# Performance work log

Hardware: AMD Instinct MI355X
Metric: run time of the kernel (lower is better)

Reference implementation:

```python
import jax, jax.numpy as jnp
import numpy as np

NUM_OCTAVES = 6
LN_EPS = 1e-5


def layer_norm(x, scale, bias):
    mu = jnp.mean(x, axis=-1, keepdims=True)
    var = jnp.var(x, axis=-1, keepdims=True)
    return (x - mu) * jax.lax.rsqrt(var + LN_EPS) * scale + bias


def bilinear_sample(img, xy):
    """torch.grid_sample(mode='bilinear', align_corners=False, padding='zeros').
    img: [B,C,H,W], xy: [B,N,2] with (x,y) in [-1,1]. Returns [B,N,C]."""
    B, C, H, W = img.shape
    ix = ((xy[..., 0] + 1.0) * W - 1.0) * 0.5  # [B,N] pixel-space x
    iy = ((xy[..., 1] + 1.0) * H - 1.0) * 0.5
    x0 = jnp.floor(ix)
    y0 = jnp.floor(iy)
    wx1 = ix - x0
    wy1 = iy - y0

    def corner(xc, yc, w):
        valid = (xc >= 0) & (xc < W) & (yc >= 0) & (yc < H)
        xi = jnp.clip(xc, 0, W - 1).astype(jnp.int32)
        yi = jnp.clip(yc, 0, H - 1).astype(jnp.int32)
        vals = jax.vmap(lambda im, a, b: im[:, a, b])(img, yi, xi)  # [B,C,N]
        return vals * (w * valid.astype(img.dtype))[:, None, :]

    out = (corner(x0, y0, (1 - wx1) * (1 - wy1))
           + corner(x0 + 1, y0, wx1 * (1 - wy1))
           + corner(x0, y0 + 1, (1 - wx1) * wy1)
           + corner(x0 + 1, y0 + 1, wx1 * wy1))
    return out.transpose(0, 2, 1)  # [B,N,C]


def pos_enc(c):
    # SRT-style positional encoding: sin/cos at octaves 2^o * pi, o in [0, NUM_OCTAVES)
    octs = (2.0 ** jnp.arange(NUM_OCTAVES)) * jnp.pi  # [O]
    s = c[..., None] * octs  # [B,N,2,O]
    B, N = c.shape[:2]
    return jnp.concatenate([jnp.sin(s).reshape(B, N, -1), jnp.cos(s).reshape(B, N, -1)], axis=-1)


def reference(image, latents, coords, ln_q_scale, ln_q_bias, ln_c_scale, ln_c_bias, w_q, w_kv, w_out, b_out):
    B, C, H, W = latents.shape
    N = coords.shape[1]  # must equal H*W when feat_unfold
    xy = jnp.flip(coords, axis=-1)  # coords.flip(-1): (row,col) -> (x,y)

    # q_features = grid_sample(latents)
    q_features = bilinear_sample(latents, xy)  # [B,N,C]

    # --- feature unfold: faithful raw reshape (B,N,C) -> (B,C,H,W) as in source ---
    uf = q_features.reshape(B, C, H, W)
    rows = jnp.arange(H)
    cols = jnp.arange(W)
    nbrs = []
    for i in (-1, 0, 1):
        for j in (-1, 0, 1):
            vr = jnp.clip(rows + i, 0, H - 1)
            vc = jnp.clip(cols + j, 0, W - 1)
            nbrs.append(uf[:, :, vr[:, None], vc[None, :]])  # [B,C,H,W]
    ctx = jnp.stack(nbrs, axis=1).reshape(B, 9, C, H * W).transpose(0, 3, 1, 2)  # [B,N,9,C]

    # --- PreNorm(Attention): per-point 1-query attention over 9-neighbor context ---
    xq = layer_norm(q_features, ln_q_scale, ln_q_bias)[:, :, None, :]  # [B,N,1,C]
    cn = layer_norm(ctx, ln_c_scale, ln_c_bias)                        # [B,N,9,C]
    q = xq @ w_q                                                       # [B,N,1,C]
    kv = cn @ w_kv                                                     # [B,N,9,2C]
    k, v = kv[..., :C], kv[..., C:]
    sim = jnp.einsum('bnqc,bnkc->bnqk', q, k) * (C ** -0.5)
    attn = jax.nn.softmax(sim, axis=-1)
    o = jnp.einsum('bnqk,bnkc->bnqc', attn, v)
    q_features = (o @ w_out + b_out)[:, :, 0, :]  # [B,N,C] (DropPath is identity at eval)

    # --- q_coords = grid_sample(make_coord grid) ---
    fy = -1.0 + (2.0 * jnp.arange(H) + 1.0) / H
    fx = -1.0 + (2.0 * jnp.arange(W) + 1.0) / W
    fcoord = jnp.stack(jnp.meshgrid(fy, fx, indexing='ij'), axis=0)  # [2,H,W]
    fcoord = jnp.broadcast_to(fcoord[None], (B, 2, H, W)).astype(latents.dtype)
    q_coords = bilinear_sample(fcoord, xy)  # [B,N,2]

    # --- q_input = grid_sample(image) ---
    q_input = bilinear_sample(image, xy)  # [B,N,1]

    pe = pos_enc((q_coords + 1.0) * 0.5)  # [B,N,4*NUM_OCTAVES]
    return jnp.concatenate([q_features, q_input, pe], axis=-1)


def setup_inputs() -> dict:
    key = jax.random.key(0)
    ks = jax.random.split(key, 8)
    B, C, H, W = 4, 64, 128, 128
    N = H * W
    image = jax.random.normal(ks[0], (B, 1, 256, 256), dtype=jnp.float32)
    latents = jax.random.normal(ks[1], (B, C, H, W), dtype=jnp.float32)
    coords = jax.random.uniform(ks[2], (B, N, 2), dtype=jnp.float32, minval=-1.0, maxval=1.0)
    w_q = jax.random.normal(ks[3], (C, C), dtype=jnp.float32) * (C ** -0.5)
    w_kv = jax.random.normal(ks[4], (C, 2 * C), dtype=jnp.float32) * (C ** -0.5)
    w_out = jax.random.normal(ks[5], (C, C), dtype=jnp.float32) * (C ** -0.5)
    return {
        'image': image, 'latents': latents, 'coords': coords,
        'ln_q_scale': jnp.ones((C,), jnp.float32), 'ln_q_bias': jnp.zeros((C,), jnp.float32),
        'ln_c_scale': jnp.ones((C,), jnp.float32), 'ln_c_bias': jnp.zeros((C,), jnp.float32),
        'w_q': w_q, 'w_kv': w_kv, 'w_out': w_out, 'b_out': jnp.zeros((C,), jnp.float32),
    }
```

## Files before the change

kernel.cpp:

```cpp
#include <hip/hip_runtime.h>
#include <cstdint>


typedef __attribute__((ext_vector_type(8))) short bf16x8;
typedef __attribute__((ext_vector_type(4))) float f32x4;
typedef __attribute__((ext_vector_type(4))) uint32_t u32x4;
typedef __attribute__((ext_vector_type(2))) uint32_t u32x2;

__device__ __forceinline__ float wsum(float v){
#pragma unroll
  for(int o=32;o>0;o>>=1) v += __shfl_xor(v,o,64);
  return v;
}
__device__ __forceinline__ unsigned short f2bf(float x){
  union{float f; uint32_t u;} c; c.f=x;
  uint32_t r = c.u + 0x7fffu + ((c.u>>16)&1u);
  return (unsigned short)(r>>16);
}
__device__ __forceinline__ float bf2f(unsigned short h){
  union{uint32_t u; float f;} c; c.u = ((uint32_t)h)<<16; return c.f;
}
__device__ __forceinline__ float blo(uint32_t u){
  union{uint32_t x; float f;} c; c.x = u<<16; return c.f;
}
__device__ __forceinline__ float bhi(uint32_t u){
  union{uint32_t x; float f;} c; c.x = u & 0xffff0000u; return c.f;
}

__global__ __launch_bounds__(256) void k_tr_bf(const float* __restrict__ in,
                                               uint16_t* __restrict__ out){
  __shared__ float t[64][65];
  const int b  = blockIdx.y;
  const int p0 = blockIdx.x * 64;
  const float* src = in  + (size_t)b * (64 * 16384);
  uint16_t*    dst = out + (size_t)b * (64 * 16384);
  const int tx = threadIdx.x & 63, ty = threadIdx.x >> 6;
#pragma unroll
  for(int j=0;j<16;j++){ int r = ty + j*4; t[r][tx] = src[(size_t)r*16384 + p0 + tx]; }
  __syncthreads();
#pragma unroll
  for(int j=0;j<16;j++){ int pr = ty + j*4; dst[(size_t)(p0+pr)*64 + tx] = f2bf(t[tx][pr]); }
}

__global__ __launch_bounds__(256) void k_sample(const uint16_t* __restrict__ lat_t,
                                                const float* __restrict__ coords,
                                                const float* __restrict__ image,
                                                const float* __restrict__ lsq,
                                                const float* __restrict__ lbq,
                                                uint16_t* __restrict__ qf,
                                                uint32_t* __restrict__ xq,
                                                float* __restrict__ out){
  const int lane = threadIdx.x & 63;
  const int pidx = blockIdx.x * 4 + (threadIdx.x >> 6);
  const int b = pidx >> 14;
  const float y = coords[(size_t)pidx*2 + 0];
  const float x = coords[(size_t)pidx*2 + 1];

  float ix = ((x + 1.f)*128.f - 1.f)*0.5f;
  float iy = ((y + 1.f)*128.f - 1.f)*0.5f;
  float x0 = floorf(ix), y0 = floorf(iy);
  float wx1 = ix - x0, wy1 = iy - y0;
  float acc = 0.f, qcy = 0.f, qcx = 0.f;
  const uint16_t* latb = lat_t + (size_t)b*16384*64;
#pragma unroll
  for(int cy=0; cy<2; cy++){
#pragma unroll
    for(int cx=0; cx<2; cx++){
      int xi = (int)x0 + cx, yi = (int)y0 + cy;
      float w = (cx ? wx1 : 1.f-wx1) * (cy ? wy1 : 1.f-wy1);
      bool valid = (xi>=0)&&(xi<128)&&(yi>=0)&&(yi<128);
      float wv = valid ? w : 0.f;
      int xc = min(max(xi,0),127), yc = min(max(yi,0),127);
      acc += wv * bf2f(latb[(size_t)(yc*128 + xc)*64 + lane]);
      qcy += wv * (-1.f + (2.f*(float)yc + 1.f)*(1.f/128.f));
      qcx += wv * (-1.f + (2.f*(float)xc + 1.f)*(1.f/128.f));
    }
  }
  qf[(size_t)pidx*64 + lane] = f2bf(acc);

  float s1 = wsum(acc), s2 = wsum(acc*acc);
  float mu = s1*(1.f/64.f);
  float rs = rsqrtf(s2*(1.f/64.f) - mu*mu + 1e-5f);
  float xv = (acc - mu)*rs*lsq[lane] + lbq[lane];
  float va = __shfl(xv, (lane&31)*2), vb = __shfl(xv, (lane&31)*2+1);
  if(lane < 32)
    xq[(size_t)pidx*32 + (lane ^ ((pidx&7)<<2))] = ((uint32_t)f2bf(vb)<<16) | f2bf(va);

  float jx = ((x + 1.f)*256.f - 1.f)*0.5f;
  float jy = ((y + 1.f)*256.f - 1.f)*0.5f;
  float jx0 = floorf(jx), jy0 = floorf(jy);
  float ux1 = jx - jx0, uy1 = jy - jy0;
  float acc2 = 0.f;
  const float* imb = image + (size_t)b*256*256;
#pragma unroll
  for(int cy=0; cy<2; cy++){
#pragma unroll
    for(int cx=0; cx<2; cx++){
      int xi = (int)jx0 + cx, yi = (int)jy0 + cy;
      float w = (cx ? ux1 : 1.f-ux1) * (cy ? uy1 : 1.f-uy1);
      bool valid = (xi>=0)&&(xi<256)&&(yi>=0)&&(yi<256);
      int xc = min(max(xi,0),255), yc = min(max(yi,0),255);
      acc2 += (valid ? w : 0.f) * imb[yc*256 + xc];
    }
  }
  size_t obase = (size_t)pidx * 89;
  if(lane == 0) out[obase + 64] = acc2;

  if(lane < 24){
    int r = (lane < 12) ? lane : lane - 12;
    int d = r / 6, o = r % 6;
    float cval = (d == 0) ? qcy : qcx;
    cval = (cval + 1.f) * 0.5f;
    float arg = cval * 3.14159265358979323846f * (float)(1 << o);
    out[obase + 65 + lane] = (lane < 12) ? sinf(arg) : cosf(arg);
  }
}

__global__ __launch_bounds__(256) void k_tr_ln(const uint16_t* __restrict__ qf,
                                               const float* __restrict__ lsc,
                                               const float* __restrict__ lbc,
                                               uint32_t* __restrict__ cn){
  __shared__ float t[64][65];
  const int b  = blockIdx.y;
  const int p0 = blockIdx.x * 64;
  const uint16_t* src = qf + (size_t)b * 1048576;
  const int tx = threadIdx.x & 63, ty = threadIdx.x >> 6;
  const float sc = lsc[tx], bc = lbc[tx];
#pragma unroll
  for(int j=0;j<16;j++){ int r = ty + j*4; t[r][tx] = bf2f(src[(size_t)r*16384 + p0 + tx]); }
  __syncthreads();
#pragma unroll
  for(int j=0;j<16;j++){
    int pr = ty + j*4;
    float v = t[tx][pr];
    float s1 = wsum(v), s2 = wsum(v*v);
    float mu = s1*(1.f/64.f);
    float rs = rsqrtf(s2*(1.f/64.f) - mu*mu + 1e-5f);
    float cv = (v - mu)*rs*sc + bc;
    float va = __shfl(cv, (tx&31)*2), vb = __shfl(cv, (tx&31)*2+1);
    int rown = p0 + pr;
    size_t row = (size_t)b*16384 + rown;
    if(tx < 32)
      cn[row*32 + (tx ^ ((rown&7)<<2))] = ((uint32_t)f2bf(vb)<<16) | f2bf(va);
  }
}

template<int MODE>
__global__ __launch_bounds__(256) void k_gemm(const uint32_t* A, const float* W,
                                              const float* bias,
                                              uint16_t* oK, uint16_t* oV, float* oF){
  constexpr int N  = (MODE==1) ? 128 : 64;
  constexpr int NT = (MODE==1) ? 2 : 1;
  __shared__ uint32_t la[128*32];
  const int t  = threadIdx.x;
  const int wv = t >> 6, ln = t & 63;
  const uint32_t* src = A + (size_t)blockIdx.x * 4096;
#pragma unroll
  for(int i=0;i<4;i++){
    *(u32x4*)&la[(i*256+t)*4] = *(const u32x4*)&src[(i*256+t)*4];
  }
  bf16x8 bfr[NT][2];
#pragma unroll
  for(int nt=0;nt<NT;nt++){
    const int ntg = wv*NT + nt;
#pragma unroll
    for(int ks=0;ks<2;ks++){
#pragma unroll
      for(int e=0;e<8;e++){
        int k = ks*32 + (ln>>4)*8 + e;
        bfr[nt][ks][e] = (short)f2bf(W[(size_t)k*N + ntg*16 + (ln&15)]);
      }
    }
  }
  __syncthreads();

  f32x4 acc[8][NT];
#pragma unroll
  for(int m=0;m<8;m++)
#pragma unroll
    for(int nt=0;nt<NT;nt++) acc[m][nt] = (f32x4){0.f,0.f,0.f,0.f};

#pragma unroll
  for(int m=0;m<8;m++){
    const int R = m*16 + (ln&15);
#pragma unroll
    for(int ks=0;ks<2;ks++){
      const int gs = (ks*4 + (ln>>4)) ^ (R&7);
      bf16x8 af = *(const bf16x8*)&la[R*32 + gs*4];
#pragma unroll
      for(int nt=0;nt<NT;nt++)
        acc[m][nt] = __builtin_amdgcn_mfma_f32_16x16x32_bf16(af, bfr[nt][ks], acc[m][nt], 0,0,0);
    }
  }

  const size_t r0 = (size_t)blockIdx.x * 128;
#pragma unroll
  for(int m=0;m<8;m++){
#pragma unroll
    for(int nt=0;nt<NT;nt++){
      const int ntg = wv*NT + nt;
      const int col = ntg*16 + (ln&15);
#pragma unroll
      for(int r=0;r<4;r++){
        const size_t row = r0 + m*16 + (ln>>4)*4 + r;
        float v = acc[m][nt][r];
        if constexpr (MODE==0){
          oK[row*64 + col] = f2bf(v * 0.125f);
        } else if constexpr (MODE==1){
          if(col < 64) oK[row*64 + col]      = f2bf(v);
          else         oV[row*64 + (col-64)] = f2bf(v);
        } else {
          oF[row*89 + col] = v + bias[col];
        }
      }
    }
  }
}

__global__ __launch_bounds__(256) void k_attn3(const uint16_t* __restrict__ Qb,
                                               const uint16_t* __restrict__ Kb,
                                               const uint16_t* __restrict__ Vb,
                                               uint32_t* __restrict__ O){
  const int t  = threadIdx.x;
  const int ln = t & 63;
  const int cl = ln & 15;
  const int p  = blockIdx.x*16 + (t>>6)*4 + (ln>>4);
  const int b = p >> 14, n = p & 16383, h = n >> 7, w = n & 127;

  u32x2 qp = *(const u32x2*)((const char*)Qb + (size_t)p*128 + cl*8);
  const float q0 = blo(qp.x), q1 = bhi(qp.x), q2 = blo(qp.y), q3 = bhi(qp.y);

  const size_t base = (size_t)b * 16384;
  float sim[9];
  uint32_t v01[9], v23[9];
#pragma unroll
  for(int k=0;k<9;k++){
    int hh = min(max(h + k/3 - 1, 0), 127);
    int ww = min(max(w + k%3 - 1, 0), 127);
    size_t pos = base + hh*128 + ww;
    u32x2 kp = *(const u32x2*)((const char*)Kb + pos*128 + cl*8);
    u32x2 vp = *(const u32x2*)((const char*)Vb + pos*128 + cl*8);
    v01[k] = vp.x; v23[k] = vp.y;
    float s = q0*blo(kp.x) + q1*bhi(kp.x) + q2*blo(kp.y) + q3*bhi(kp.y);
#pragma unroll
    for(int o=8;o>0;o>>=1) s += __shfl_xor(s, o, 64);
    sim[k] = s;
  }
  float m = sim[0];
#pragma unroll
  for(int k=1;k<9;k++) m = fmaxf(m, sim[k]);
  float se = 0.f, o0 = 0.f, o1 = 0.f, o2 = 0.f, o3 = 0.f;
#pragma unroll
  for(int k=0;k<9;k++){
    float e = __expf(sim[k] - m);
    se += e;
    o0 += e*blo(v01[k]); o1 += e*bhi(v01[k]);
    o2 += e*blo(v23[k]); o3 += e*bhi(v23[k]);
  }
  float inv = 1.f/se;
  o0 *= inv; o1 *= inv; o2 *= inv; o3 *= inv;
  const uint32_t w01 = ((uint32_t)f2bf(o1)<<16) | f2bf(o0);
  const uint32_t w23 = ((uint32_t)f2bf(o3)<<16) | f2bf(o2);
  const int key = (p&7)<<2;
  O[(size_t)p*32 + ((cl*2  ) ^ key)] = w01;
  O[(size_t)p*32 + ((cl*2+1) ^ key)] = w23;
}

extern "C" void kernel_launch(void* const* d_in, const int* in_sizes, int n_in,
                              void* d_out, int out_size, void* d_ws, size_t ws_size,
                              hipStream_t stream){
  const float* image   = (const float*)d_in[0];
  const float* latents = (const float*)d_in[1];
  const float* coords  = (const float*)d_in[2];
  const float* lsq     = (const float*)d_in[3];
  const float* lbq     = (const float*)d_in[4];
  const float* lsc     = (const float*)d_in[5];
  const float* lbc     = (const float*)d_in[6];
  const float* wq      = (const float*)d_in[7];
  const float* wkv     = (const float*)d_in[8];
  const float* wout    = (const float*)d_in[9];
  const float* bout    = (const float*)d_in[10];
  float* out = (float*)d_out;

  char* ws = (char*)d_ws;
  uint16_t* latT = (uint16_t*)ws;
  uint32_t* CN   = (uint32_t*)ws;
  uint16_t* Kb   = (uint16_t*)ws;
  uint16_t* Vb   = (uint16_t*)(ws + 8388608);
  uint16_t* qfB  = (uint16_t*)(ws + 16777216);
  uint32_t* O    = (uint32_t*)(ws + 16777216);
  uint32_t* XQ   = (uint32_t*)(ws + 25165824);
  uint16_t* Qb   = (uint16_t*)(ws + 25165824);

  dim3 trg(256, 4);
  k_tr_bf <<<trg,   256, 0, stream>>>(latents, latT);
  k_sample<<<16384, 256, 0, stream>>>(latT, coords, image, lsq, lbq, qfB, XQ, out);
  k_tr_ln <<<trg,   256, 0, stream>>>(qfB, lsc, lbc, CN);
  k_gemm<0><<<512,  256, 0, stream>>>(XQ, wq,  nullptr, Qb, nullptr, nullptr);
  k_gemm<1><<<512,  256, 0, stream>>>(CN, wkv, nullptr, Kb, Vb,      nullptr);
  k_attn3 <<<4096,  256, 0, stream>>>(Qb, Kb, Vb, O);
  k_gemm<2><<<512,  256, 0, stream>>>(O, wout, bout, nullptr, nullptr, out);
}
```

Before: 168.9 us.

## Fuse context layernorm with Q/KV projections and attention with output projection

Merges the transpose+LayerNorm kernel and the two projection GEMMs into one kernel that keeps the normalized context and query tiles in shared memory. It also merges the 3x3 neighborhood attention with the output projection, so the attention result stays in LDS instead of going through global memory. This cuts the pipeline from seven launches to four and removes the CN and O intermediate round trips. The trade-off is larger shared-memory footprint, more registers per block and fewer blocks for the attention stage, since 512 blocks of 512 threads replace 4096 blocks of 256.

```diff
diff --git a/kernel.cpp b/kernel.cpp
--- a/kernel.cpp
+++ b/kernel.cpp
@@ -4,6 +4,7 @@
 
 typedef __attribute__((ext_vector_type(8))) short bf16x8;
 typedef __attribute__((ext_vector_type(4))) float f32x4;
+typedef __attribute__((ext_vector_type(2))) float f32x2;
 typedef __attribute__((ext_vector_type(4))) uint32_t u32x4;
 typedef __attribute__((ext_vector_type(2))) uint32_t u32x2;
 
@@ -116,154 +117,245 @@
   }
 }
 
-__global__ __launch_bounds__(256) void k_tr_ln(const uint16_t* __restrict__ qf,
-                                               const float* __restrict__ lsc,
-                                               const float* __restrict__ lbc,
-                                               uint32_t* __restrict__ cn){
-  __shared__ float t[64][65];
-  const int b  = blockIdx.y;
-  const int p0 = blockIdx.x * 64;
-  const uint16_t* src = qf + (size_t)b * 1048576;
-  const int tx = threadIdx.x & 63, ty = threadIdx.x >> 6;
-  const float sc = lsc[tx], bc = lbc[tx];
-#pragma unroll
-  for(int j=0;j<16;j++){ int r = ty + j*4; t[r][tx] = bf2f(src[(size_t)r*16384 + p0 + tx]); }
-  __syncthreads();
-#pragma unroll
-  for(int j=0;j<16;j++){
-    int pr = ty + j*4;
-    float v = t[tx][pr];
-    float s1 = wsum(v), s2 = wsum(v*v);
-    float mu = s1*(1.f/64.f);
-    float rs = rsqrtf(s2*(1.f/64.f) - mu*mu + 1e-5f);
-    float cv = (v - mu)*rs*sc + bc;
-    float va = __shfl(cv, (tx&31)*2), vb = __shfl(cv, (tx&31)*2+1);
-    int rown = p0 + pr;
-    size_t row = (size_t)b*16384 + rown;
-    if(tx < 32)
-      cn[row*32 + (tx ^ ((rown&7)<<2))] = ((uint32_t)f2bf(vb)<<16) | f2bf(va);
-  }
-}
-
-template<int MODE>
-__global__ __launch_bounds__(256) void k_gemm(const uint32_t* A, const float* W,
-                                              const float* bias,
-                                              uint16_t* oK, uint16_t* oV, float* oF){
-  constexpr int N  = (MODE==1) ? 128 : 64;
-  constexpr int NT = (MODE==1) ? 2 : 1;
-  __shared__ uint32_t la[128*32];
+__global__ __launch_bounds__(256) void k_proj(const uint16_t* __restrict__ qf,
+                                              const uint32_t* __restrict__ XQ,
+                                              const float* __restrict__ lsc,
+                                              const float* __restrict__ lbc,
+                                              const float* __restrict__ wq,
+                                              const float* __restrict__ wkv,
+                                              uint16_t* __restrict__ Qb,
+                                              uint16_t* __restrict__ Kb,
+                                              uint16_t* __restrict__ Vb){
+  __shared__ float tile[64][130];
+  __shared__ uint32_t Acn[128*32];
+  uint32_t* Axq = (uint32_t*)&tile[0][0];
+
+  const int t   = threadIdx.x;
+  const int blk = blockIdx.x;
+  const int b   = blk >> 7;
+  const int P0  = (blk & 127) * 128;
+  const uint16_t* src = qf + (size_t)b*1048576;
+
+  {
+    const int r = t >> 2, q4 = t & 3;
+    const uint16_t* rp = src + (size_t)r*16384 + P0 + q4*32;
+#pragma unroll
+    for(int i=0;i<4;i++){
+      u32x4 raw = *(const u32x4*)(rp + i*8);
+#pragma unroll
+      for(int j=0;j<4;j++){
+        *(f32x2*)&tile[r][q4*32 + i*8 + j*2] = (f32x2){blo(raw[j]), bhi(raw[j])};
+      }
+    }
+  }
+  __syncthreads();
+
+  {
+    const int tx = t & 63, ty = t >> 6;
+    const float sc = lsc[tx], bc = lbc[tx];
+#pragma unroll
+    for(int j=0;j<32;j++){
+      int pr = ty + j*4;
+      float v = tile[tx][pr];
+      float s1 = wsum(v), s2 = wsum(v*v);
+      float mu = s1*(1.f/64.f);
+      float rs = rsqrtf(s2*(1.f/64.f) - mu*mu + 1e-5f);
+      float cv = (v - mu)*rs*sc + bc;
+      float va = __shfl(cv, (tx&31)*2), vb = __shfl(cv, (tx&31)*2+1);
+      if(tx < 32)
+        Acn[pr*32 + (tx ^ ((pr&7)<<2))] = ((uint32_t)f2bf(vb)<<16) | f2bf(va);
+    }
+  }
+  __syncthreads();
+
+  {
+    const uint32_t* xsrc = XQ + (size_t)blk * 4096;
+#pragma unroll
+    for(int i=0;i<4;i++)
+      *(u32x4*)&Axq[(i*256 + t)*4] = *(const u32x4*)&xsrc[(i*256 + t)*4];
+  }
+  __syncthreads();
+
+  const int wv = t >> 6, ln = t & 63;
+  const size_t r0 = (size_t)blk * 128;
+
+  {
+    bf16x8 wf[4][2];
+#pragma unroll
+    for(int nt=0;nt<4;nt++)
+#pragma unroll
+      for(int ks=0;ks<2;ks++)
+#pragma unroll
+        for(int e=0;e<8;e++){
+          int k = ks*32 + (ln>>4)*8 + e;
+          wf[nt][ks][e] = (short)f2bf(wq[(size_t)k*64 + nt*16 + (ln&15)]);
+        }
+    f32x4 acc[2][4];
+#pragma unroll
+    for(int mi=0;mi<2;mi++)
+#pragma unroll
+      for(int nt=0;nt<4;nt++) acc[mi][nt] = (f32x4){0.f,0.f,0.f,0.f};
+#pragma unroll
+    for(int mi=0;mi<2;mi++){
+      const int m = wv + mi*4;
+      const int R = m*16 + (ln&15);
+#pragma unroll
+      for(int ks=0;ks<2;ks++){
+        bf16x8 af = *(const bf16x8*)&Axq[R*32 + (((ks*4 + (ln>>4)) ^ (R&7))*4)];
+#pragma unroll
+        for(int nt=0;nt<4;nt++)
+          acc[mi][nt] = __builtin_amdgcn_mfma_f32_16x16x32_bf16(af, wf[nt][ks], acc[mi][nt], 0,0,0);
+      }
+    }
+#pragma unroll
+    for(int mi=0;mi<2;mi++){
+      const int m = wv + mi*4;
+#pragma unroll
+      for(int nt=0;nt<4;nt++){
+        const int col = nt*16 + (ln&15);
+#pragma unroll
+        for(int r=0;r<4;r++){
+          const size_t row = r0 + m*16 + (ln>>4)*4 + r;
+          Qb[row*64 + col] = f2bf(acc[mi][nt][r]*0.125f);
+        }
+      }
+    }
+  }
+
+  {
+    bf16x8 wf[8][2];
+#pragma unroll
+    for(int nt=0;nt<8;nt++)
+#pragma unroll
+      for(int ks=0;ks<2;ks++)
+#pragma unroll
+        for(int e=0;e<8;e++){
+          int k = ks*32 + (ln>>4)*8 + e;
+          wf[nt][ks][e] = (short)f2bf(wkv[(size_t)k*128 + nt*16 + (ln&15)]);
+        }
+    f32x4 acc[2][8];
+#pragma unroll
+    for(int mi=0;mi<2;mi++)
+#pragma unroll
+      for(int nt=0;nt<8;nt++) acc[mi][nt] = (f32x4){0.f,0.f,0.f,0.f};
+#pragma unroll
+    for(int mi=0;mi<2;mi++){
+      const int m = wv + mi*4;
+      const int R = m*16 + (ln&15);
+#pragma unroll
+      for(int ks=0;ks<2;ks++){
+        bf16x8 af = *(const bf16x8*)&Acn[R*32 + (((ks*4 + (ln>>4)) ^ (R&7))*4)];
+#pragma unroll
+        for(int nt=0;nt<8;nt++)
+          acc[mi][nt] = __builtin_amdgcn_mfma_f32_16x16x32_bf16(af, wf[nt][ks], acc[mi][nt], 0,0,0);
+      }
+    }
+#pragma unroll
+    for(int mi=0;mi<2;mi++){
+      const int m = wv + mi*4;
+#pragma unroll
+      for(int nt=0;nt<8;nt++){
+        const int col = nt*16 + (ln&15);
+#pragma unroll
+        for(int r=0;r<4;r++){
+          const size_t row = r0 + m*16 + (ln>>4)*4 + r;
+          float v = acc[mi][nt][r];
+          if(col < 64) Kb[row*64 + col]      = f2bf(v);
+          else         Vb[row*64 + (col-64)] = f2bf(v);
+        }
+      }
+    }
+  }
+}
+
+__global__ __launch_bounds__(512) void k_attn_out(const uint16_t* __restrict__ Qb,
+                                                  const uint16_t* __restrict__ Kb,
+                                                  const uint16_t* __restrict__ Vb,
+                                                  const float* __restrict__ wout,
+                                                  const float* __restrict__ bout,
+                                                  float* __restrict__ out){
+  __shared__ uint32_t Ot[128*32];
   const int t  = threadIdx.x;
   const int wv = t >> 6, ln = t & 63;
-  const uint32_t* src = A + (size_t)blockIdx.x * 4096;
-#pragma unroll
-  for(int i=0;i<4;i++){
-    *(u32x4*)&la[(i*256+t)*4] = *(const u32x4*)&src[(i*256+t)*4];
-  }
-  bf16x8 bfr[NT][2];
-#pragma unroll
-  for(int nt=0;nt<NT;nt++){
-    const int ntg = wv*NT + nt;
-#pragma unroll
-    for(int ks=0;ks<2;ks++){
+  const int blk = blockIdx.x;
+  const int b = blk >> 7, h = blk & 127;
+  const size_t base = (size_t)b * 16384;
+  const size_t p0   = base + (size_t)h * 128;
+
+  const int cl = ln & 15;
+#pragma unroll
+  for(int it=0; it<4; it++){
+    const int local = wv*16 + it*4 + (ln>>4);
+    const size_t p = p0 + local;
+    u32x2 qp = *(const u32x2*)((const char*)Qb + p*128 + cl*8);
+    const float q0 = blo(qp.x), q1 = bhi(qp.x), q2 = blo(qp.y), q3 = bhi(qp.y);
+
+    float sim[9];
+    uint32_t v01[9], v23[9];
+#pragma unroll
+    for(int k=0;k<9;k++){
+      int hh = min(max(h + k/3 - 1, 0), 127);
+      int ww = min(max(local + k%3 - 1, 0), 127);
+      size_t pos = base + hh*128 + ww;
+      u32x2 kp = *(const u32x2*)((const char*)Kb + pos*128 + cl*8);
+      u32x2 vp = *(const u32x2*)((const char*)Vb + pos*128 + cl*8);
+      v01[k] = vp.x; v23[k] = vp.y;
+      float s = q0*blo(kp.x) + q1*bhi(kp.x) + q2*blo(kp.y) + q3*bhi(kp.y);
+#pragma unroll
+      for(int o=8;o>0;o>>=1) s += __shfl_xor(s, o, 64);
+      sim[k] = s;
+    }
+    float m = sim[0];
+#pragma unroll
+    for(int k=1;k<9;k++) m = fmaxf(m, sim[k]);
+    float se = 0.f, o0 = 0.f, o1 = 0.f, o2 = 0.f, o3 = 0.f;
+#pragma unroll
+    for(int k=0;k<9;k++){
+      float e = __expf(sim[k] - m);
+      se += e;
+      o0 += e*blo(v01[k]); o1 += e*bhi(v01[k]);
+      o2 += e*blo(v23[k]); o3 += e*bhi(v23[k]);
+    }
+    float inv = 1.f/se;
+    const uint32_t w01 = ((uint32_t)f2bf(o1*inv)<<16) | f2bf(o0*inv);
+    const uint32_t w23 = ((uint32_t)f2bf(o3*inv)<<16) | f2bf(o2*inv);
+    const int key = (local&7)<<2;
+    Ot[local*32 + ((cl*2  ) ^ key)] = w01;
+    Ot[local*32 + ((cl*2+1) ^ key)] = w23;
+  }
+  __syncthreads();
+
+  bf16x8 wf[4][2];
+#pragma unroll
+  for(int nt=0;nt<4;nt++)
+#pragma unroll
+    for(int ks=0;ks<2;ks++)
 #pragma unroll
       for(int e=0;e<8;e++){
         int k = ks*32 + (ln>>4)*8 + e;
-        bfr[nt][ks][e] = (short)f2bf(W[(size_t)k*N + ntg*16 + (ln&15)]);
-      }
-    }
-  }
-  __syncthreads();
-
-  f32x4 acc[8][NT];
-#pragma unroll
-  for(int m=0;m<8;m++)
-#pragma unroll
-    for(int nt=0;nt<NT;nt++) acc[m][nt] = (f32x4){0.f,0.f,0.f,0.f};
-
-#pragma unroll
-  for(int m=0;m<8;m++){
-    const int R = m*16 + (ln&15);
-#pragma unroll
-    for(int ks=0;ks<2;ks++){
-      const int gs = (ks*4 + (ln>>4)) ^ (R&7);
-      bf16x8 af = *(const bf16x8*)&la[R*32 + gs*4];
-#pragma unroll
-      for(int nt=0;nt<NT;nt++)
-        acc[m][nt] = __builtin_amdgcn_mfma_f32_16x16x32_bf16(af, bfr[nt][ks], acc[m][nt], 0,0,0);
-    }
-  }
-
-  const size_t r0 = (size_t)blockIdx.x * 128;
-#pragma unroll
-  for(int m=0;m<8;m++){
-#pragma unroll
-    for(int nt=0;nt<NT;nt++){
-      const int ntg = wv*NT + nt;
-      const int col = ntg*16 + (ln&15);
-#pragma unroll
-      for(int r=0;r<4;r++){
-        const size_t row = r0 + m*16 + (ln>>4)*4 + r;
-        float v = acc[m][nt][r];
-        if constexpr (MODE==0){
-          oK[row*64 + col] = f2bf(v * 0.125f);
-        } else if constexpr (MODE==1){
-          if(col < 64) oK[row*64 + col]      = f2bf(v);
-          else         oV[row*64 + (col-64)] = f2bf(v);
-        } else {
-          oF[row*89 + col] = v + bias[col];
-        }
-      }
-    }
-  }
-}
-
-__global__ __launch_bounds__(256) void k_attn3(const uint16_t* __restrict__ Qb,
-                                               const uint16_t* __restrict__ Kb,
-                                               const uint16_t* __restrict__ Vb,
-                                               uint32_t* __restrict__ O){
-  const int t  = threadIdx.x;
-  const int ln = t & 63;
-  const int cl = ln & 15;
-  const int p  = blockIdx.x*16 + (t>>6)*4 + (ln>>4);
-  const int b = p >> 14, n = p & 16383, h = n >> 7, w = n & 127;
-
-  u32x2 qp = *(const u32x2*)((const char*)Qb + (size_t)p*128 + cl*8);
-  const float q0 = blo(qp.x), q1 = bhi(qp.x), q2 = blo(qp.y), q3 = bhi(qp.y);
-
-  const size_t base = (size_t)b * 16384;
-  float sim[9];
-  uint32_t v01[9], v23[9];
-#pragma unroll
-  for(int k=0;k<9;k++){
-    int hh = min(max(h + k/3 - 1, 0), 127);
-    int ww = min(max(w + k%3 - 1, 0), 127);
-    size_t pos = base + hh*128 + ww;
-    u32x2 kp = *(const u32x2*)((const char*)Kb + pos*128 + cl*8);
-    u32x2 vp = *(const u32x2*)((const char*)Vb + pos*128 + cl*8);
-    v01[k] = vp.x; v23[k] = vp.y;
-    float s = q0*blo(kp.x) + q1*bhi(kp.x) + q2*blo(kp.y) + q3*bhi(kp.y);
-#pragma unroll
-    for(int o=8;o>0;o>>=1) s += __shfl_xor(s, o, 64);
-    sim[k] = s;
-  }
-  float m = sim[0];
-#pragma unroll
-  for(int k=1;k<9;k++) m = fmaxf(m, sim[k]);
-  float se = 0.f, o0 = 0.f, o1 = 0.f, o2 = 0.f, o3 = 0.f;
-#pragma unroll
-  for(int k=0;k<9;k++){
-    float e = __expf(sim[k] - m);
-    se += e;
-    o0 += e*blo(v01[k]); o1 += e*bhi(v01[k]);
-    o2 += e*blo(v23[k]); o3 += e*bhi(v23[k]);
-  }
-  float inv = 1.f/se;
-  o0 *= inv; o1 *= inv; o2 *= inv; o3 *= inv;
-  const uint32_t w01 = ((uint32_t)f2bf(o1)<<16) | f2bf(o0);
-  const uint32_t w23 = ((uint32_t)f2bf(o3)<<16) | f2bf(o2);
-  const int key = (p&7)<<2;
-  O[(size_t)p*32 + ((cl*2  ) ^ key)] = w01;
-  O[(size_t)p*32 + ((cl*2+1) ^ key)] = w23;
+        wf[nt][ks][e] = (short)f2bf(wout[(size_t)k*64 + nt*16 + (ln&15)]);
+      }
+  f32x4 acc[4];
+#pragma unroll
+  for(int nt=0;nt<4;nt++) acc[nt] = (f32x4){0.f,0.f,0.f,0.f};
+  const int R = wv*16 + (ln&15);
+#pragma unroll
+  for(int ks=0;ks<2;ks++){
+    bf16x8 af = *(const bf16x8*)&Ot[R*32 + (((ks*4 + (ln>>4)) ^ (R&7))*4)];
+#pragma unroll
+    for(int nt=0;nt<4;nt++)
+      acc[nt] = __builtin_amdgcn_mfma_f32_16x16x32_bf16(af, wf[nt][ks], acc[nt], 0,0,0);
+  }
+#pragma unroll
+  for(int nt=0;nt<4;nt++){
+    const int col = nt*16 + (ln&15);
+    const float bb = bout[col];
+#pragma unroll
+    for(int r=0;r<4;r++){
+      const size_t row = p0 + wv*16 + (ln>>4)*4 + r;
+      out[row*89 + col] = acc[nt][r] + bb;
+    }
+  }
 }
 
 extern "C" void kernel_launch(void* const* d_in, const int* in_sizes, int n_in,
@@ -284,20 +376,15 @@
 
   char* ws = (char*)d_ws;
   uint16_t* latT = (uint16_t*)ws;
-  uint32_t* CN   = (uint32_t*)ws;
   uint16_t* Kb   = (uint16_t*)ws;
   uint16_t* Vb   = (uint16_t*)(ws + 8388608);
   uint16_t* qfB  = (uint16_t*)(ws + 16777216);
-  uint32_t* O    = (uint32_t*)(ws + 16777216);
   uint32_t* XQ   = (uint32_t*)(ws + 25165824);
   uint16_t* Qb   = (uint16_t*)(ws + 25165824);
 
   dim3 trg(256, 4);
-  k_tr_bf <<<trg,   256, 0, stream>>>(latents, latT);
-  k_sample<<<16384, 256, 0, stream>>>(latT, coords, image, lsq, lbq, qfB, XQ, out);
-  k_tr_ln <<<trg,   256, 0, stream>>>(qfB, lsc, lbc, CN);
-  k_gemm<0><<<512,  256, 0, stream>>>(XQ, wq,  nullptr, Qb, nullptr, nullptr);
-  k_gemm<1><<<512,  256, 0, stream>>>(CN, wkv, nullptr, Kb, Vb,      nullptr);
-  k_attn3 <<<4096,  256, 0, stream>>>(Qb, Kb, Vb, O);
-  k_gemm<2><<<512,  256, 0, stream>>>(O, wout, bout, nullptr, nullptr, out);
-}
+  k_tr_bf   <<<trg,   256, 0, stream>>>(latents, latT);
+  k_sample  <<<16384, 256, 0, stream>>>(latT, coords, image, lsq, lbq, qfB, XQ, out);
+  k_proj    <<<512,   256, 0, stream>>>(qfB, XQ, lsc, lbc, wq, wkv, Qb, Kb, Vb);
+  k_attn_out<<<512,   512, 0, stream>>>(Qb, Kb, Vb, wout, bout, out);
+}
```

Result: faster. 158.7 us (-6.1%).
